# Kernel optimization log

Hardware: AMD Instinct MI355X
Metric: run time of the kernel (lower is better)

Reference implementation:

```python
import jax, jax.numpy as jnp
import numpy as np

B, D, H = 1024, 64, 128


def setup_inputs() -> dict:
    key = jax.random.key(0)
    ks = jax.random.split(key, 12)
    s1 = 1.0 / np.sqrt(4 * D)
    sh = 1.0 / np.sqrt(H)
    sd = 1.0 / np.sqrt(D)
    return {
        "x": jax.random.normal(ks[0], (B, D), dtype=jnp.float32),
        # edge_fn: Linear(4D,H) -> ReLU -> Linear(H,H)
        "W1": jax.random.uniform(ks[1], (4 * D, H), minval=-s1, maxval=s1, dtype=jnp.float32),
        "b1": jax.random.uniform(ks[2], (H,), minval=-s1, maxval=s1, dtype=jnp.float32),
        "W2": jax.random.uniform(ks[3], (H, H), minval=-sh, maxval=sh, dtype=jnp.float32),
        "b2": jax.random.uniform(ks[4], (H,), minval=-sh, maxval=sh, dtype=jnp.float32),
        # tau_proj: Linear(D,1) -> Softplus
        "Wt": jax.random.uniform(ks[5], (D, 1), minval=-sd, maxval=sd, dtype=jnp.float32),
        "bt": jax.random.uniform(ks[6], (1,), minval=-sd, maxval=sd, dtype=jnp.float32),
        # agg: Linear(H,H) -> ReLU
        "Wa": jax.random.uniform(ks[7], (H, H), minval=-sh, maxval=sh, dtype=jnp.float32),
        "ba": jax.random.uniform(ks[8], (H,), minval=-sh, maxval=sh, dtype=jnp.float32),
        # res_proj: Linear(D,H)
        "Wr": jax.random.uniform(ks[9], (D, H), minval=-sd, maxval=sd, dtype=jnp.float32),
        "br": jax.random.uniform(ks[10], (H,), minval=-sd, maxval=sd, dtype=jnp.float32),
        # LayerNorm(H)
        "gamma": jnp.ones((H,), dtype=jnp.float32),
        "beta": jnp.zeros((H,), dtype=jnp.float32),
    }


def reference(x, W1, b1, W2, b2, Wt, bt, Wa, ba, Wr, br, gamma, beta):
    d = x.shape[1]
    # Decompose first linear over concat([x_i, x_j, delta, |delta|]) into 4 sub-matmuls;
    # only the |delta| term needs the pairwise [B,B,D] tensor.
    Wi, Wj, Wd, Wab = W1[:d], W1[d:2 * d], W1[2 * d:3 * d], W1[3 * d:]
    ti = x @ Wi            # [B,H] (i-dependent)
    tj = x @ Wj            # [B,H] (j-dependent)
    td = x @ Wd            # [B,H] (delta = x_i - x_j contribution)
    delta = x[:, None, :] - x[None, :, :]             # [B,B,D]
    ta = jnp.einsum('ijd,dh->ijh', jnp.abs(delta), Wab)  # [B,B,H]
    pre = ti[:, None, :] + tj[None, :, :] + td[:, None, :] - td[None, :, :] + ta + b1
    d_proj = jax.nn.relu(pre) @ W2 + b2               # [B,B,H]
    tau = jnp.maximum(jax.nn.softplus(x @ Wt + bt), 0.01) + 1.0  # [B,1]
    h_mean = d_proj.mean(axis=1) / tau                # mean over j
    h = jax.nn.relu(h_mean @ Wa + ba)
    y = h + (x @ Wr + br)
    mu = y.mean(axis=-1, keepdims=True)
    var = ((y - mu) ** 2).mean(axis=-1, keepdims=True)  # biased, like torch LayerNorm
    return (y - mu) * jax.lax.rsqrt(var + 1e-5) * gamma + beta
```

## Files before the change

### kernel.cpp

```cpp
#include <hip/hip_runtime.h>
#include <hip/hip_bf16.h>
#include <math.h>

#define BB 1024
#define DD 64
#define HH 128

typedef _Float16 half8 __attribute__((ext_vector_type(8)));
typedef __fp16 fp16x2 __attribute__((ext_vector_type(2)));
typedef float floatx4 __attribute__((ext_vector_type(4)));

union H8 { fp16x2 p[4]; half8 v; };

__device__ __forceinline__ void async_cp16(const float* g, float* lds_wave_base) {
    __builtin_amdgcn_global_load_lds(
        (const __attribute__((address_space(1))) unsigned int*)g,
        (__attribute__((address_space(3))) unsigned int*)lds_wave_base,
        16, 0, 0);
}

__global__ __launch_bounds__(256) void prep_kernel(
    const float* __restrict__ x, const float* __restrict__ W1,
    const float* __restrict__ b1,
    float* __restrict__ c1, float* __restrict__ c2P,
    _Float16* __restrict__ wpack)
{
    __shared__ float xs[2][DD];
    const int t = threadIdx.x;
    const int i0 = blockIdx.x * 2;
    if (t < 128) xs[t >> 6][t & 63] = x[i0 * DD + t];
    __syncthreads();

    const int ii = t >> 7;
    const int h = t & 127;
    const int i = i0 + ii;

    if (blockIdx.y == 0) {
        float a1 = 0.f;
        #pragma unroll 8
        for (int k = 0; k < DD; k++) {
            float wi = W1[k * HH + h];
            float wd = W1[(2 * DD + k) * HH + h];
            a1 = fmaf(xs[ii][k], wi + wd, a1);
        }
        c1[i * HH + h] = a1 + b1[h];
    } else {
        float a2 = 0.f;
        #pragma unroll 8
        for (int k = 0; k < DD; k++) {
            float wj = W1[(DD + k) * HH + h];
            float wd = W1[(2 * DD + k) * HH + h];
            a2 = fmaf(xs[ii][k], wj - wd, a2);
        }
        c2P[(i >> 4) * 2048 + (h >> 6) * 1024 + ((h >> 4) & 3) * 256
            + ((i & 15) >> 2) * 64 + (h & 15) * 4 + (i & 3)] = a2;

        if (blockIdx.x < 32) {
            int f = blockIdx.x * 256 + t;
            int jj = f & 7;
            int l  = (f >> 3) & 63;
            int u  = f >> 9;
            int s  = u & 1, t4 = (u >> 1) & 3, hh = u >> 3;
            int k  = s * 32 + ((l >> 4) << 3) + jj;
            int hcol = hh * 64 + t4 * 16 + (l & 15);
            wpack[f] = (_Float16)W1[(3 * DD + k) * HH + hcol];
        }
    }
}

__global__ __launch_bounds__(256, 4) void pair_kernel(
    const float* __restrict__ x, const float* __restrict__ c1,
    const float* __restrict__ c2P, const _Float16* __restrict__ wpack,
    float* __restrict__ Sp)
{
    __shared__ __align__(16) float xs[2][1024];
    __shared__ __align__(16) float c2s[2][1024];

    const int t = threadIdx.x;
    const int wave = t >> 6;
    const int l = t & 63;
    const int quad = l >> 4, lm = l & 15;
    const int bid = blockIdx.x;
    const int ig = bid >> 3;
    const int hh = (bid >> 2) & 1;
    const int jq = bid & 3;
    const int i = ig * 4 + wave;
    const int j0base = jq * 256;
    const int sw = lm & 7;

    async_cp16(x + (j0base + (t >> 4)) * DD + (((t & 15) ^ ((t >> 4) & 7)) << 2),
               &xs[0][0] + wave * 256);
    async_cp16(c2P + (j0base >> 4) * 2048 + hh * 1024 + t * 4,
               &c2s[0][0] + wave * 256);

    float xi[16];
    {
        const float* xg = x + i * DD + quad * 8;
        *(float4*)(xi)      = *(const float4*)(xg);
        *(float4*)(xi + 4)  = *(const float4*)(xg + 4);
        *(float4*)(xi + 8)  = *(const float4*)(xg + 32);
        *(float4*)(xi + 12) = *(const float4*)(xg + 36);
    }
    float c1r[4];
    #pragma unroll
    for (int t4 = 0; t4 < 4; t4++)
        c1r[t4] = c1[i * HH + hh * 64 + t4 * 16 + lm];
    half8 wf[8];
    #pragma unroll
    for (int u = 0; u < 8; u++)
        wf[u] = *(const half8*)(wpack + ((hh * 8 + u) * 64 + l) * 8);

    float S[4] = {0.f, 0.f, 0.f, 0.f};

    for (int tile = 0; tile < 16; ++tile) {
        const int cur = tile & 1;
        __syncthreads();

        if (tile < 15) {
            const int jn = j0base + (tile + 1) * 16;
            async_cp16(x + (jn + (t >> 4)) * DD + (((t & 15) ^ ((t >> 4) & 7)) << 2),
                       &xs[cur ^ 1][0] + wave * 256);
            async_cp16(c2P + (jn >> 4) * 2048 + hh * 1024 + t * 4,
                       &c2s[cur ^ 1][0] + wave * 256);
        }

        floatx4 acc[4];
        #pragma unroll
        for (int t4 = 0; t4 < 4; t4++) {
            float4 c2v = *(const float4*)(&c2s[cur][t4 * 256 + l * 4]);
            acc[t4][0] = c2v.x + c1r[t4];
            acc[t4][1] = c2v.y + c1r[t4];
            acc[t4][2] = c2v.z + c1r[t4];
            acc[t4][3] = c2v.w + c1r[t4];
        }

        const float* xb = &xs[cur][lm * 64];
        float4 a0 = *(const float4*)(xb + (((quad * 2)     ^ sw) << 2));
        float4 a1 = *(const float4*)(xb + (((quad * 2 + 1) ^ sw) << 2));
        float4 a2 = *(const float4*)(xb + (((quad * 2 + 8) ^ sw) << 2));
        float4 a3 = *(const float4*)(xb + (((quad * 2 + 9) ^ sw) << 2));
        H8 af0, af1;
        af0.p[0] = __builtin_amdgcn_cvt_pkrtz(fabsf(xi[0] - a0.x),  fabsf(xi[1] - a0.y));
        af0.p[1] = __builtin_amdgcn_cvt_pkrtz(fabsf(xi[2] - a0.z),  fabsf(xi[3] - a0.w));
        af0.p[2] = __builtin_amdgcn_cvt_pkrtz(fabsf(xi[4] - a1.x),  fabsf(xi[5] - a1.y));
        af0.p[3] = __builtin_amdgcn_cvt_pkrtz(fabsf(xi[6] - a1.z),  fabsf(xi[7] - a1.w));
        af1.p[0] = __builtin_amdgcn_cvt_pkrtz(fabsf(xi[8] - a2.x),  fabsf(xi[9] - a2.y));
        af1.p[1] = __builtin_amdgcn_cvt_pkrtz(fabsf(xi[10] - a2.z), fabsf(xi[11] - a2.w));
        af1.p[2] = __builtin_amdgcn_cvt_pkrtz(fabsf(xi[12] - a3.x), fabsf(xi[13] - a3.y));
        af1.p[3] = __builtin_amdgcn_cvt_pkrtz(fabsf(xi[14] - a3.z), fabsf(xi[15] - a3.w));

        #pragma unroll
        for (int t4 = 0; t4 < 4; t4++) {
            acc[t4] = __builtin_amdgcn_mfma_f32_16x16x32_f16(af0.v, wf[t4 * 2 + 0], acc[t4], 0, 0, 0);
            acc[t4] = __builtin_amdgcn_mfma_f32_16x16x32_f16(af1.v, wf[t4 * 2 + 1], acc[t4], 0, 0, 0);
        }
        #pragma unroll
        for (int t4 = 0; t4 < 4; t4++) {
            S[t4] += fmaxf(acc[t4][0], 0.f);
            S[t4] += fmaxf(acc[t4][1], 0.f);
            S[t4] += fmaxf(acc[t4][2], 0.f);
            S[t4] += fmaxf(acc[t4][3], 0.f);
        }
    }

    #pragma unroll
    for (int t4 = 0; t4 < 4; t4++) {
        S[t4] += __shfl_xor(S[t4], 16, 64);
        S[t4] += __shfl_xor(S[t4], 32, 64);
    }
    if (quad == 0) {
        #pragma unroll
        for (int t4 = 0; t4 < 4; t4++)
            Sp[(jq * BB + i) * HH + hh * 64 + t4 * 16 + lm] = S[t4];
    }
}

__global__ __launch_bounds__(128) void finish_kernel(
    const float* __restrict__ Sp, const float* __restrict__ W2,
    const float* __restrict__ b2, const float* __restrict__ x,
    const float* __restrict__ Wt, const float* __restrict__ bt,
    const float* __restrict__ Wa, const float* __restrict__ ba,
    const float* __restrict__ Wr, const float* __restrict__ br,
    const float* __restrict__ gamma, const float* __restrict__ beta,
    float* __restrict__ out)
{
    __shared__ float Srow[HH];
    __shared__ float mrow[HH];
    __shared__ float xrow[DD];
    __shared__ float red[2][2];
    __shared__ float tau_s;
    const int t = threadIdx.x;
    const int h = t;
    const int wv = t >> 6;
    const int l = t & 63;
    const int i = blockIdx.x;

    {
        float s = 0.f;
        #pragma unroll
        for (int q = 0; q < 4; q++)
            s += Sp[(q * BB + i) * HH + h];
        Srow[h] = s * (1.0f / (float)BB);
    }
    if (wv == 0) {
        float xv = x[i * DD + l];
        xrow[l] = xv;
        float p = xv * Wt[l];
        #pragma unroll
        for (int off = 32; off; off >>= 1) p += __shfl_xor(p, off, 64);
        if (l == 0) {
            float z = p + bt[0];
            float sp = (z > 20.f) ? z : log1pf(expf(z));
            tau_s = fmaxf(sp, 0.01f) + 1.0f;
        }
    }
    __syncthreads();

    float acc = b2[h];
    #pragma unroll 8
    for (int k = 0; k < HH; k++)
        acc = fmaf(Srow[k], W2[k * HH + h], acc);
    const float itau = 1.0f / tau_s;
    mrow[h] = acc * itau;
    __syncthreads();

    float a2 = ba[h];
    #pragma unroll 8
    for (int k = 0; k < HH; k++)
        a2 = fmaf(mrow[k], Wa[k * HH + h], a2);
    float y = fmaxf(a2, 0.f) + br[h];
    #pragma unroll 8
    for (int d = 0; d < DD; d++)
        y = fmaf(xrow[d], Wr[d * HH + h], y);

    float p = y;
    #pragma unroll
    for (int off = 32; off; off >>= 1) p += __shfl_xor(p, off, 64);
    if (l == 0) red[0][wv] = p;
    __syncthreads();
    float mu = (red[0][0] + red[0][1]) * (1.0f / (float)HH);
    float dy = y - mu;
    float q = dy * dy;
    #pragma unroll
    for (int off = 32; off; off >>= 1) q += __shfl_xor(q, off, 64);
    if (l == 0) red[1][wv] = q;
    __syncthreads();
    float rs = rsqrtf((red[1][0] + red[1][1]) * (1.0f / (float)HH) + 1e-5f);
    out[i * HH + h] = dy * rs * gamma[h] + beta[h];
}

extern "C" void kernel_launch(void* const* d_in, const int* in_sizes, int n_in,
                              void* d_out, int out_size, void* d_ws, size_t ws_size,
                              hipStream_t stream)
{
    const float* x     = (const float*)d_in[0];
    const float* W1    = (const float*)d_in[1];
    const float* b1    = (const float*)d_in[2];
    const float* W2    = (const float*)d_in[3];
    const float* b2    = (const float*)d_in[4];
    const float* Wt    = (const float*)d_in[5];
    const float* bt    = (const float*)d_in[6];
    const float* Wa    = (const float*)d_in[7];
    const float* ba    = (const float*)d_in[8];
    const float* Wr    = (const float*)d_in[9];
    const float* br    = (const float*)d_in[10];
    const float* gamma = (const float*)d_in[11];
    const float* beta  = (const float*)d_in[12];
    float* out = (float*)d_out;

    char* ws = (char*)d_ws;
    float*     c1    = (float*)(ws);
    float*     c2P   = (float*)(ws + (512 << 10));
    _Float16*  wpack = (_Float16*)(ws + (1024 << 10));
    float*     Sp    = (float*)(ws + (1056 << 10));

    prep_kernel<<<dim3(512, 2), 256, 0, stream>>>(x, W1, b1, c1, c2P, wpack);
    pair_kernel<<<2048, 256, 0, stream>>>(x, c1, c2P, wpack, Sp);
    finish_kernel<<<1024, 128, 0, stream>>>(Sp, W2, b2, x, Wt, bt,
                                            Wa, ba, Wr, br, gamma, beta, out);
}
```

Measured before the change: 127.9 us.

## Process two i rows per wave and hoist c1 bias out of relu loop

Each wave now computes two i rows against the same j tile, reusing the LDS x_j and c2 loads and the packed W fragments across both. The c1 bias is removed from the per-tile accumulator init by using max(acc, -c1) and adding 64*c1 once after the loop. Grid size halves and the occupancy hint drops to 3 blocks, trading parallelism and register pressure for less LDS traffic per MFMA.

```diff
diff --git a/kernel.cpp b/kernel.cpp
--- a/kernel.cpp
+++ b/kernel.cpp
@@ -68,7 +68,7 @@
     }
 }
 
-__global__ __launch_bounds__(256, 4) void pair_kernel(
+__global__ __launch_bounds__(256, 3) void pair_kernel(
     const float* __restrict__ x, const float* __restrict__ c1,
     const float* __restrict__ c2P, const _Float16* __restrict__ wpack,
     float* __restrict__ Sp)
@@ -84,7 +84,8 @@
     const int ig = bid >> 3;
     const int hh = (bid >> 2) & 1;
     const int jq = bid & 3;
-    const int i = ig * 4 + wave;
+    const int iA = ig * 8 + wave * 2;
+    const int iB = iA + 1;
     const int j0base = jq * 256;
     const int sw = lm & 7;
 
@@ -93,24 +94,32 @@
     async_cp16(c2P + (j0base >> 4) * 2048 + hh * 1024 + t * 4,
                &c2s[0][0] + wave * 256);
 
-    float xi[16];
+    float xiA[16], xiB[16];
     {
-        const float* xg = x + i * DD + quad * 8;
-        *(float4*)(xi)      = *(const float4*)(xg);
-        *(float4*)(xi + 4)  = *(const float4*)(xg + 4);
-        *(float4*)(xi + 8)  = *(const float4*)(xg + 32);
-        *(float4*)(xi + 12) = *(const float4*)(xg + 36);
-    }
-    float c1r[4];
-    #pragma unroll
-    for (int t4 = 0; t4 < 4; t4++)
-        c1r[t4] = c1[i * HH + hh * 64 + t4 * 16 + lm];
+        const float* xg = x + iA * DD + quad * 8;
+        *(float4*)(xiA)      = *(const float4*)(xg);
+        *(float4*)(xiA + 4)  = *(const float4*)(xg + 4);
+        *(float4*)(xiA + 8)  = *(const float4*)(xg + 32);
+        *(float4*)(xiA + 12) = *(const float4*)(xg + 36);
+        const float* xh = x + iB * DD + quad * 8;
+        *(float4*)(xiB)      = *(const float4*)(xh);
+        *(float4*)(xiB + 4)  = *(const float4*)(xh + 4);
+        *(float4*)(xiB + 8)  = *(const float4*)(xh + 32);
+        *(float4*)(xiB + 12) = *(const float4*)(xh + 36);
+    }
+    float c1A[4], c1B[4];
+    #pragma unroll
+    for (int t4 = 0; t4 < 4; t4++) {
+        c1A[t4] = c1[iA * HH + hh * 64 + t4 * 16 + lm];
+        c1B[t4] = c1[iB * HH + hh * 64 + t4 * 16 + lm];
+    }
     half8 wf[8];
     #pragma unroll
     for (int u = 0; u < 8; u++)
         wf[u] = *(const half8*)(wpack + ((hh * 8 + u) * 64 + l) * 8);
 
-    float S[4] = {0.f, 0.f, 0.f, 0.f};
+    float SA[4] = {0.f, 0.f, 0.f, 0.f};
+    float SB[4] = {0.f, 0.f, 0.f, 0.f};
 
     for (int tile = 0; tile < 16; ++tile) {
         const int cur = tile & 1;
@@ -124,54 +133,86 @@
                        &c2s[cur ^ 1][0] + wave * 256);
         }
 
-        floatx4 acc[4];
-        #pragma unroll
-        for (int t4 = 0; t4 < 4; t4++) {
-            float4 c2v = *(const float4*)(&c2s[cur][t4 * 256 + l * 4]);
-            acc[t4][0] = c2v.x + c1r[t4];
-            acc[t4][1] = c2v.y + c1r[t4];
-            acc[t4][2] = c2v.z + c1r[t4];
-            acc[t4][3] = c2v.w + c1r[t4];
-        }
-
         const float* xb = &xs[cur][lm * 64];
         float4 a0 = *(const float4*)(xb + (((quad * 2)     ^ sw) << 2));
         float4 a1 = *(const float4*)(xb + (((quad * 2 + 1) ^ sw) << 2));
         float4 a2 = *(const float4*)(xb + (((quad * 2 + 8) ^ sw) << 2));
         float4 a3 = *(const float4*)(xb + (((quad * 2 + 9) ^ sw) << 2));
-        H8 af0, af1;
-        af0.p[0] = __builtin_amdgcn_cvt_pkrtz(fabsf(xi[0] - a0.x),  fabsf(xi[1] - a0.y));
-        af0.p[1] = __builtin_amdgcn_cvt_pkrtz(fabsf(xi[2] - a0.z),  fabsf(xi[3] - a0.w));
-        af0.p[2] = __builtin_amdgcn_cvt_pkrtz(fabsf(xi[4] - a1.x),  fabsf(xi[5] - a1.y));
-        af0.p[3] = __builtin_amdgcn_cvt_pkrtz(fabsf(xi[6] - a1.z),  fabsf(xi[7] - a1.w));
-        af1.p[0] = __builtin_amdgcn_cvt_pkrtz(fabsf(xi[8] - a2.x),  fabsf(xi[9] - a2.y));
-        af1.p[1] = __builtin_amdgcn_cvt_pkrtz(fabsf(xi[10] - a2.z), fabsf(xi[11] - a2.w));
-        af1.p[2] = __builtin_amdgcn_cvt_pkrtz(fabsf(xi[12] - a3.x), fabsf(xi[13] - a3.y));
-        af1.p[3] = __builtin_amdgcn_cvt_pkrtz(fabsf(xi[14] - a3.z), fabsf(xi[15] - a3.w));
-
+
+        H8 afA0, afA1, afB0, afB1;
+        afA0.p[0] = __builtin_amdgcn_cvt_pkrtz(fabsf(xiA[0] - a0.x),  fabsf(xiA[1] - a0.y));
+        afA0.p[1] = __builtin_amdgcn_cvt_pkrtz(fabsf(xiA[2] - a0.z),  fabsf(xiA[3] - a0.w));
+        afA0.p[2] = __builtin_amdgcn_cvt_pkrtz(fabsf(xiA[4] - a1.x),  fabsf(xiA[5] - a1.y));
+        afA0.p[3] = __builtin_amdgcn_cvt_pkrtz(fabsf(xiA[6] - a1.z),  fabsf(xiA[7] - a1.w));
+        afA1.p[0] = __builtin_amdgcn_cvt_pkrtz(fabsf(xiA[8] - a2.x),  fabsf(xiA[9] - a2.y));
+        afA1.p[1] = __builtin_amdgcn_cvt_pkrtz(fabsf(xiA[10] - a2.z), fabsf(xiA[11] - a2.w));
+        afA1.p[2] = __builtin_amdgcn_cvt_pkrtz(fabsf(xiA[12] - a3.x), fabsf(xiA[13] - a3.y));
+        afA1.p[3] = __builtin_amdgcn_cvt_pkrtz(fabsf(xiA[14] - a3.z), fabsf(xiA[15] - a3.w));
+        afB0.p[0] = __builtin_amdgcn_cvt_pkrtz(fabsf(xiB[0] - a0.x),  fabsf(xiB[1] - a0.y));
+        afB0.p[1] = __builtin_amdgcn_cvt_pkrtz(fabsf(xiB[2] - a0.z),  fabsf(xiB[3] - a0.w));
+        afB0.p[2] = __builtin_amdgcn_cvt_pkrtz(fabsf(xiB[4] - a1.x),  fabsf(xiB[5] - a1.y));
+        afB0.p[3] = __builtin_amdgcn_cvt_pkrtz(fabsf(xiB[6] - a1.z),  fabsf(xiB[7] - a1.w));
+        afB1.p[0] = __builtin_amdgcn_cvt_pkrtz(fabsf(xiB[8] - a2.x),  fabsf(xiB[9] - a2.y));
+        afB1.p[1] = __builtin_amdgcn_cvt_pkrtz(fabsf(xiB[10] - a2.z), fabsf(xiB[11] - a2.w));
+        afB1.p[2] = __builtin_amdgcn_cvt_pkrtz(fabsf(xiB[12] - a3.x), fabsf(xiB[13] - a3.y));
+        afB1.p[3] = __builtin_amdgcn_cvt_pkrtz(fabsf(xiB[14] - a3.z), fabsf(xiB[15] - a3.w));
+
+        {
+            floatx4 acc[4];
+            #pragma unroll
+            for (int t4 = 0; t4 < 4; t4++)
+                acc[t4] = *(const floatx4*)(&c2s[cur][t4 * 256 + l * 4]);
+            #pragma unroll
+            for (int t4 = 0; t4 < 4; t4++) {
+                acc[t4] = __builtin_amdgcn_mfma_f32_16x16x32_f16(afA0.v, wf[t4 * 2 + 0], acc[t4], 0, 0, 0);
+                acc[t4] = __builtin_amdgcn_mfma_f32_16x16x32_f16(afA1.v, wf[t4 * 2 + 1], acc[t4], 0, 0, 0);
+            }
+            #pragma unroll
+            for (int t4 = 0; t4 < 4; t4++) {
+                SA[t4] += fmaxf(acc[t4][0], -c1A[t4]);
+                SA[t4] += fmaxf(acc[t4][1], -c1A[t4]);
+                SA[t4] += fmaxf(acc[t4][2], -c1A[t4]);
+                SA[t4] += fmaxf(acc[t4][3], -c1A[t4]);
+            }
+        }
+        {
+            floatx4 acc[4];
+            #pragma unroll
+            for (int t4 = 0; t4 < 4; t4++)
+                acc[t4] = *(const floatx4*)(&c2s[cur][t4 * 256 + l * 4]);
+            #pragma unroll
+            for (int t4 = 0; t4 < 4; t4++) {
+                acc[t4] = __builtin_amdgcn_mfma_f32_16x16x32_f16(afB0.v, wf[t4 * 2 + 0], acc[t4], 0, 0, 0);
+                acc[t4] = __builtin_amdgcn_mfma_f32_16x16x32_f16(afB1.v, wf[t4 * 2 + 1], acc[t4], 0, 0, 0);
+            }
+            #pragma unroll
+            for (int t4 = 0; t4 < 4; t4++) {
+                SB[t4] += fmaxf(acc[t4][0], -c1B[t4]);
+                SB[t4] += fmaxf(acc[t4][1], -c1B[t4]);
+                SB[t4] += fmaxf(acc[t4][2], -c1B[t4]);
+                SB[t4] += fmaxf(acc[t4][3], -c1B[t4]);
+            }
+        }
+    }
+
+    #pragma unroll
+    for (int t4 = 0; t4 < 4; t4++) {
+        SA[t4] = fmaf(64.f, c1A[t4], SA[t4]);
+        SB[t4] = fmaf(64.f, c1B[t4], SB[t4]);
+    }
+    #pragma unroll
+    for (int t4 = 0; t4 < 4; t4++) {
+        SA[t4] += __shfl_xor(SA[t4], 16, 64);
+        SA[t4] += __shfl_xor(SA[t4], 32, 64);
+        SB[t4] += __shfl_xor(SB[t4], 16, 64);
+        SB[t4] += __shfl_xor(SB[t4], 32, 64);
+    }
+    if (quad == 0) {
         #pragma unroll
         for (int t4 = 0; t4 < 4; t4++) {
-            acc[t4] = __builtin_amdgcn_mfma_f32_16x16x32_f16(af0.v, wf[t4 * 2 + 0], acc[t4], 0, 0, 0);
-            acc[t4] = __builtin_amdgcn_mfma_f32_16x16x32_f16(af1.v, wf[t4 * 2 + 1], acc[t4], 0, 0, 0);
-        }
-        #pragma unroll
-        for (int t4 = 0; t4 < 4; t4++) {
-            S[t4] += fmaxf(acc[t4][0], 0.f);
-            S[t4] += fmaxf(acc[t4][1], 0.f);
-            S[t4] += fmaxf(acc[t4][2], 0.f);
-            S[t4] += fmaxf(acc[t4][3], 0.f);
-        }
-    }
-
-    #pragma unroll
-    for (int t4 = 0; t4 < 4; t4++) {
-        S[t4] += __shfl_xor(S[t4], 16, 64);
-        S[t4] += __shfl_xor(S[t4], 32, 64);
-    }
-    if (quad == 0) {
-        #pragma unroll
-        for (int t4 = 0; t4 < 4; t4++)
-            Sp[(jq * BB + i) * HH + hh * 64 + t4 * 16 + lm] = S[t4];
+            Sp[(jq * BB + iA) * HH + hh * 64 + t4 * 16 + lm] = SA[t4];
+            Sp[(jq * BB + iB) * HH + hh * 64 + t4 * 16 + lm] = SB[t4];
+        }
     }
 }
 
@@ -275,7 +316,7 @@
     float*     Sp    = (float*)(ws + (1056 << 10));
 
     prep_kernel<<<dim3(512, 2), 256, 0, stream>>>(x, W1, b1, c1, c2P, wpack);
-    pair_kernel<<<2048, 256, 0, stream>>>(x, c1, c2P, wpack, Sp);
+    pair_kernel<<<1024, 256, 0, stream>>>(x, c1, c2P, wpack, Sp);
     finish_kernel<<<1024, 128, 0, stream>>>(Sp, W2, b2, x, Wt, bt,
                                             Wa, ba, Wr, br, gamma, beta, out);
 }
```

Result: no change. 126.6 us (-1.0%).
